# Performance work log

Hardware: AMD Instinct MI355X
Metric: run time of the kernel (lower is better)

The kernel has to match this reference:

```python
import jax, jax.numpy as jnp
import numpy as np

B, S, D, H = 4, 1024, 1024, 16
HD = D // H  # per-head dim = 64
NEG = -10000000000.0


def setup_inputs() -> dict:
    key = jax.random.key(0)
    ks = jax.random.split(key, 12)
    q = jax.random.normal(ks[0], (B, S, D), jnp.float32)
    k = jax.random.normal(ks[1], (B, S, D), jnp.float32)
    v = jax.random.normal(ks[2], (B, S, D), jnp.float32)
    mask = jax.random.randint(ks[3], (B, S, S), 0, 2).astype(jnp.int32)
    sc = 1.0 / np.sqrt(D)
    Wq = jax.random.normal(ks[4], (H, D, HD), jnp.float32) * sc
    bq = jnp.zeros((H, HD), jnp.float32)
    Wk = jax.random.normal(ks[5], (H, D, HD), jnp.float32) * sc
    bk = jnp.zeros((H, HD), jnp.float32)
    Wv = jax.random.normal(ks[6], (H, D, HD), jnp.float32) * sc
    bv = jnp.zeros((H, HD), jnp.float32)
    Wo = jax.random.normal(ks[7], (D, D), jnp.float32) * sc
    bo = jnp.zeros((D,), jnp.float32)
    return {"query": q, "key": k, "value": v, "attention_mask": mask,
            "Wq": Wq, "bq": bq, "Wk": Wk, "bk": bk, "Wv": Wv, "bv": bv,
            "Wo": Wo, "bo": bo}


def reference(query, key, value, attention_mask, Wq, bq, Wk, bk, Wv, bv, Wo, bo):
    # batched per-head projections: [B,S,D] x [H,D,E] -> [B,H,S,E]
    q = jnp.einsum('bsd,hde->bhse', query, Wq) + bq[None, :, None, :]
    k = jnp.einsum('bsd,hde->bhse', key, Wk) + bk[None, :, None, :]
    v = jnp.einsum('bsd,hde->bhse', value, Wv) + bv[None, :, None, :]
    # NOTE: scale uses key_dim (model_size = full D), faithful to source
    score = jnp.einsum('bhse,bhte->bhst', q, k) / jnp.sqrt(jnp.float32(D))
    m = attention_mask.astype(jnp.float32)[:, None, :, :]  # [B,1,S,S]
    score = score + (1.0 - m) * NEG
    attn = jax.nn.softmax(score, axis=-1) * m  # double masking
    heads = jnp.einsum('bhst,bhte->bhse', attn, v)  # [B,H,S,E]
    # concat heads along feature dim (head order preserved)
    heads = heads.transpose(0, 2, 1, 3).reshape(B, S, D)
    return heads @ Wo + bo
```

## Files before the change

### kernel.cpp

```cpp
#include <hip/hip_runtime.h>

#define B_ 4
#define S_ 1024
#define D_ 1024
#define H_ 16
#define E_ 64
#define BS_ (B_*S_)
#define BHSE_ (B_*H_*S_*E_)

typedef __attribute__((ext_vector_type(8))) short bf16x8;
typedef __attribute__((ext_vector_type(4))) float f32x4;
typedef __attribute__((ext_vector_type(4))) unsigned int u32x4;

__device__ __forceinline__ unsigned short f2bf(float f) {
    unsigned int x = __float_as_uint(f);
    x = (x + 0x7FFFu + ((x >> 16) & 1u)) >> 16;
    return (unsigned short)x;
}
__device__ __forceinline__ float bf2f(unsigned short u) {
    return __uint_as_float(((unsigned int)u) << 16);
}
__device__ __forceinline__ float ldin(const void* p, size_t i, int isb) {
    return isb ? bf2f(((const unsigned short*)p)[i]) : ((const float*)p)[i];
}

__device__ __forceinline__ unsigned int cvtpk(float lo, float hi) {
    unsigned int r;
    asm("v_cvt_pk_bf16_f32 %0, %1, %2" : "=v"(r) : "v"(lo), "v"(hi));
    return r;
}
__device__ __forceinline__ unsigned int bperm(int srclane4, unsigned int v) {
    return (unsigned int)__builtin_amdgcn_ds_bpermute(srclane4, (int)v);
}
__device__ __forceinline__ bf16x8 u4bf(u32x4 w) {
    union { u32x4 u; bf16x8 h; } c; c.u = w; return c.h;
}

#if __has_builtin(__builtin_amdgcn_exp2f)
#define EXP2(x) __builtin_amdgcn_exp2f(x)
#else
#define EXP2(x) __expf((x) * 0.6931471805599453f)
#endif

__device__ __forceinline__ void gl2lds16(const void* g, void* l) {
    __builtin_amdgcn_global_load_lds(
        (const __attribute__((address_space(1))) void*)g,
        (__attribute__((address_space(3))) void*)l, 16, 0, 0);
}

__device__ __forceinline__ int detect_isb(const unsigned int* q) {
    unsigned int wv = q[threadIdx.x & 63];
    unsigned int lo = wv & 0xFFFFu;
    unsigned int e = (lo >> 7) & 0xFFu;
    int ok = (lo == 0u) || (e >= 100u && e <= 145u);
    return __popcll(__ballot(ok)) >= 48;
}

__global__ __launch_bounds__(256) void preproc(
        const void* q_, const void* k_, const void* v_, const int* mask,
        const void* Wq, const void* Wk, const void* Wv, const void* Wo,
        const void* bq_, const void* bk_, const void* bv_, const void* bo_,
        unsigned short* WT, float* biases, unsigned long long* packT,
        unsigned short* Aconv) {
    __shared__ unsigned short Tt[64][72];
    const int isb = detect_isb((const unsigned int*)q_);
    const int blk = blockIdx.x, t = threadIdx.x;

    if (blk < 1024) {
        const int c0 = blk & 15, r0 = ((blk >> 4) & 15) * 64, z = blk >> 8;
        const void* src = (z == 0) ? Wq : (z == 1) ? Wk : (z == 2) ? Wv : Wo;
        {
            int dl = t >> 2, qc = t & 3;
            size_t base;
            if (z < 3) base = (size_t)c0 * 65536 + (size_t)(r0 + dl) * 64 + qc * 16;
            else       base = (size_t)(r0 + dl) * 1024 + (size_t)c0 * 64 + qc * 16;
            if (isb) {
                const unsigned short* s = (const unsigned short*)src + base;
                bf16x8 a0 = *(const bf16x8*)s, a1 = *(const bf16x8*)(s + 8);
#pragma unroll
                for (int j = 0; j < 8; j++) {
                    Tt[qc * 16 + j][dl] = (unsigned short)a0[j];
                    Tt[qc * 16 + 8 + j][dl] = (unsigned short)a1[j];
                }
            } else {
                const float* s = (const float*)src + base;
#pragma unroll
                for (int j = 0; j < 16; j++) Tt[qc * 16 + j][dl] = f2bf(s[j]);
            }
        }
        __syncthreads();
        {
            int el = t >> 2, qc = t & 3;
            size_t dst = (size_t)z * D_ * D_ + (size_t)(c0 * 64 + el) * D_ + r0 + qc * 16;
            *(bf16x8*)&WT[dst]     = *(const bf16x8*)&Tt[el][qc * 16];
            *(bf16x8*)&WT[dst + 8] = *(const bf16x8*)&Tt[el][qc * 16 + 8];
        }
        if (z == 3 && ((blk >> 4) & 15) == 0 && c0 < 4) {
            const void* bs = (c0 == 0) ? bq_ : (c0 == 1) ? bk_
                           : (c0 == 2) ? bv_ : bo_;
#pragma unroll
            for (int j = 0; j < 4; j++) {
                int i = t * 4 + j;
                biases[c0 * 1024 + i] = ldin(bs, i, isb);
            }
        }
    } else if (blk < 5120) {
        int unit = (blk - 1024) * 4 + (t >> 6);
        int lane = t & 63;
        int b = unit >> 12, rem = unit & 4095, s0 = (rem >> 4) * 4, kt = rem & 15;
        const int* mb = mask + ((size_t)b * 1024 + s0) * 1024 + kt * 64 + lane;
        unsigned long long bits[4];
#pragma unroll
        for (int j = 0; j < 4; j++) bits[j] = __ballot(mb[j * 1024] != 0);
        if (lane < 4) {
            unsigned long long bb = (lane == 0) ? bits[0] : (lane == 1) ? bits[1]
                                  : (lane == 2) ? bits[2] : bits[3];
            packT[((size_t)b * 16 + kt) * 1024 + s0 + lane] = bb;
        }
    } else {
        if (isb) return;
        int blk2 = blk - 5120;
        const int z = blk2 >> 11;
        const float* s = (z == 0) ? (const float*)q_ : (z == 1) ? (const float*)k_
                                                                : (const float*)v_;
        const size_t i = ((size_t)(blk2 & 2047) * 256 + t) * 8;
        f32x4 a0 = *(const f32x4*)(s + i);
        f32x4 a1 = *(const f32x4*)(s + i + 4);
        bf16x8 o;
#pragma unroll
        for (int j = 0; j < 4; j++) {
            o[j]     = (short)f2bf(a0[j]);
            o[4 + j] = (short)f2bf(a1[j]);
        }
        *(bf16x8*)&Aconv[(size_t)z * ((size_t)BS_ * D_) + i] = o;
    }
}

template<int BM, int BN, int MODE, int MINW>
__global__ __launch_bounds__(256, MINW) void gemm_k(
        const void* A0, const void* A1, const void* A2, const unsigned short* Aconv,
        const unsigned short* BtB, const float* biasB, void* dstB,
        const unsigned int* qdet) {
    constexpr int TOT16 = (BM + BN) * 32;
    constexpr int CALLS = TOT16 / 512;
    constexpr int CPW = CALLS / 4;
    constexpr int MT = BM / 32;
    constexpr int NT = BN / 32;
    __shared__ unsigned short buf[3][TOT16];

    const int fl = detect_isb(qdet);
    const int t = threadIdx.x, lane = t & 63, w = t >> 6;
    const int lm = lane & 15, q4 = lane >> 4;
    const int wm = w >> 1, wn = w & 1;
    const int lr = lane >> 2;
    const int ls = lane & 3;
    const int lg = ls ^ ((lr >> 1) & 3);

    const unsigned short* Abf;
    const unsigned short* Bt;
    const float* bias;
    int z = 0, m0, n0, phase;
    if (MODE == 0) {
        int bid = blockIdx.x + gridDim.x * (blockIdx.y + gridDim.y * blockIdx.z);
        int xcd = bid & 7, idx = bid >> 3;
        z = idx >> 5;
        int r = idx & 31;
        int mt = (xcd << 2) + (r & 3);
        int nt = r >> 2;
        m0 = mt * BM; n0 = nt * BN;
        phase = (nt * 13 + z * 5) & 31;
        const void* Ain = (z == 0) ? A0 : (z == 1 ? A1 : A2);
        Abf = fl ? (const unsigned short*)Ain
                 : Aconv + (size_t)z * ((size_t)BS_ * D_);
        Bt = BtB + (size_t)z * D_ * D_;
        bias = biasB + z * 1024;
    } else {
        Abf = (const unsigned short*)A0;
        Bt = BtB; bias = biasB;
        int bid = blockIdx.x + (blockIdx.y << 5);
        int xcd = bid & 7, idx = bid >> 3;
        m0 = ((xcd << 2) + (idx & 3)) * BM;
        n0 = (idx >> 2) * BN;
        phase = ((idx >> 2) * 13) & 31;
    }

    auto stage = [&](int kk, int bi) {
#pragma unroll
        for (int i = 0; i < CPW; ++i) {
            int c = w * CPW + i;
            int row = c * 16 + lr;
            const unsigned short* g;
            if (row < BM)
                g = Abf + (size_t)(m0 + row) * D_ + kk + lg * 8;
            else
                g = Bt + (size_t)(n0 + row - BM) * D_ + kk + lg * 8;
            gl2lds16(g, &buf[bi][c * 512]);
        }
    };

    f32x4 acc[MT][NT];
#pragma unroll
    for (int i = 0; i < MT; i++)
#pragma unroll
        for (int j = 0; j < NT; j++) acc[i][j] = (f32x4){0.f, 0.f, 0.f, 0.f};

    stage((phase & 31) * 32, 0);
    stage(((1 + phase) & 31) * 32, 1);
    for (int it = 0; it < D_ / 32; ++it) {
        const int bi = it % 3;
        if (it < D_ / 32 - 1) {
            asm volatile("s_waitcnt vmcnt(%0)" :: "n"(CPW) : "memory");
        } else {
            asm volatile("s_waitcnt vmcnt(0)" ::: "memory");
        }
        __builtin_amdgcn_s_barrier();
        __builtin_amdgcn_sched_barrier(0);
        if (it < D_ / 32 - 2) stage(((it + 2 + phase) & 31) * 32, (it + 2) % 3);

        const unsigned short* As = buf[bi];
        const unsigned short* Bs = buf[bi] + BM * 32;
        bf16x8 af[MT], bv[NT];
#pragma unroll
        for (int mt = 0; mt < MT; mt++) {
            int row = wm * (BM / 2) + mt * 16 + lm;
            af[mt] = *(const bf16x8*)&As[row * 32 + (q4 ^ ((row >> 1) & 3)) * 8];
        }
#pragma unroll
        for (int nt = 0; nt < NT; nt++) {
            int row = wn * (BN / 2) + nt * 16 + lm;
            bv[nt] = *(const bf16x8*)&Bs[row * 32 + (q4 ^ ((row >> 1) & 3)) * 8];
        }
#pragma unroll
        for (int mt = 0; mt < MT; mt++)
#pragma unroll
            for (int nt = 0; nt < NT; nt++)
                acc[mt][nt] = __builtin_amdgcn_mfma_f32_16x16x32_bf16(
                    af[mt], bv[nt], acc[mt][nt], 0, 0, 0);
    }

#pragma unroll
    for (int mt = 0; mt < MT; mt++)
#pragma unroll
        for (int nt = 0; nt < NT; nt++) {
            int N = n0 + wn * (BN / 2) + nt * 16 + lm;
            int Mb = m0 + wm * (BM / 2) + mt * 16 + q4 * 4;
            if (MODE == 0 && z == 2) {
                int bb = Mb >> 10, sb = Mb & 1023, hh = N >> 6, e = N & 63;
                unsigned long long hv = 0;
#pragma unroll
                for (int r = 0; r < 4; r++)
                    hv |= (unsigned long long)f2bf(acc[mt][nt][r] + bias[N]) << (16 * r);
                unsigned short* d16 = (unsigned short*)dstB + (size_t)2 * BHSE_;
                *(unsigned long long*)&d16[(((size_t)(bb * H_ + hh) * E_ + e) << 10) + sb] = hv;
            } else {
#pragma unroll
                for (int r = 0; r < 4; r++) {
                    int M = Mb + r;
                    float v = acc[mt][nt][r] + bias[N];
                    if (MODE == 0) {
                        int bb = M >> 10, s = M & 1023, hh = N >> 6, e = N & 63;
                        unsigned short* d16 = (unsigned short*)dstB + (size_t)z * BHSE_;
                        d16[((size_t)(bb * H_ + hh) * S_ + s) * E_ + e] = f2bf(v);
                    } else {
                        size_t idx = (size_t)M * D_ + N;
                        if (fl) ((unsigned short*)dstB)[idx] = f2bf(v);
                        else    ((float*)dstB)[idx] = v;
                    }
                }
            }
        }
}

__global__ __launch_bounds__(1024, 4) void attn64(
        const unsigned short* Qp, const unsigned short* Kp, const unsigned short* VpT,
        const unsigned long long* packT, unsigned short* heads) {
    __shared__ unsigned short KT[2][16384];
    __shared__ unsigned short VT[2][16384];

    const int bid = blockIdx.x + (blockIdx.y << 2) + (blockIdx.z << 6);
    const int xcd = bid & 7, idx = bid >> 3;
    const int qt = idx >> 3;
    const int hb = xcd * 8 + (idx & 7);
    const int h = hb & 15, b = hb >> 4;

    const int t = threadIdx.x, w = t >> 6, lane = t & 63, lm = lane & 15, q4 = lane >> 4;
    const size_t bh = ((size_t)b * H_ + h) * S_ * E_;
    const unsigned short* Qb = Qp + bh;
    const unsigned short* Kb = Kp + bh;
    const unsigned short* Vb = VpT + bh;
    const int q0 = qt * 256 + w * 16;

    const int l3 = lane >> 3, l7 = lane & 7;
    const int kLaneOff = l3 * 64 + (l7 ^ l3) * 8;
    const int vLaneOff = l3 * 1024 + (l7 ^ l3) * 8;

    const int sw = lm & 7;
    const int c0 = (q4 ^ sw) * 8, c1 = ((q4 ^ 4) ^ sw) * 8;

    const int srcA4 = ((lane & 15) | ((lane & 16) << 1)) << 2;
    const int srcB4 = srcA4 + 64;
    const bool selHi = (lane & 32) != 0;

    bf16x8 bq0 = *(const bf16x8*)&Qb[(size_t)(q0 + lm) * E_ + q4 * 8];
    bf16x8 bq1 = *(const bf16x8*)&Qb[(size_t)(q0 + lm) * E_ + 32 + q4 * 8];

    bf16x8 ones;
#pragma unroll
    for (int j = 0; j < 8; j++) ones[j] = (short)0x3F80;

    f32x4 oacc[4];
#pragma unroll
    for (int i = 0; i < 4; i++) oacc[i] = (f32x4){0.f, 0.f, 0.f, 0.f};
    f32x4 accL = (f32x4){0.f, 0.f, 0.f, 0.f};
    float mrun = -3.0e38f;
    const float scale2 = 0.03125f * 1.4426950408889634f;

#define STAGE(tile, bufi)                                                     \
    {                                                                         \
        int k0s = (tile) * 256;                                               \
        _Pragma("unroll")                                                     \
        for (int i_ = 0; i_ < 4; ++i_) {                                      \
            int c_ = w * 4 + i_;                                              \
            if (c_ < 32) {                                                    \
                gl2lds16(Kb + (size_t)k0s * 64 + c_ * 512 + kLaneOff,         \
                         &KT[bufi][c_ * 512]);                                \
            } else {                                                          \
                int cc_ = c_ - 32, sub_ = cc_ >> 3, ec_ = cc_ & 7;            \
                gl2lds16(Vb + (size_t)ec_ * 8192 + k0s + sub_ * 64 + vLaneOff,\
                         &VT[bufi][sub_ * 4096 + ec_ * 512]);                 \
            }                                                                 \
        }                                                                     \
    }

    STAGE(0, 0)
    unsigned long long mk[4], mkn[4];
#pragma unroll
    for (int j = 0; j < 4; j++)
        mk[j] = packT[((size_t)b * 16 + j) * 1024 + q0 + lm];

    for (int T = 0; T < S_ / 256; ++T) {
        const int bufi = T & 1;
        __syncthreads();
        if (T < 3) {
            STAGE(T + 1, bufi ^ 1)
#pragma unroll
            for (int j = 0; j < 4; j++)
                mkn[j] = packT[((size_t)b * 16 + 4 * T + 4 + j) * 1024 + q0 + lm];
        }

#pragma unroll
        for (int half = 0; half < 2; ++half) {
            f32x4 st[2][4];
            __builtin_amdgcn_s_setprio(1);
#pragma unroll
            for (int sub = 0; sub < 2; ++sub)
#pragma unroll
                for (int jt = 0; jt < 4; ++jt) {
                    const unsigned short* kr =
                        &KT[bufi][(half * 128 + sub * 64 + jt * 16 + lm) * 64];
                    bf16x8 ka0 = *(const bf16x8*)&kr[c0];
                    bf16x8 ka1 = *(const bf16x8*)&kr[c1];
                    f32x4 zz = (f32x4){0.f, 0.f, 0.f, 0.f};
                    zz = __builtin_amdgcn_mfma_f32_16x16x32_bf16(ka0, bq0, zz, 0, 0, 0);
                    zz = __builtin_amdgcn_mfma_f32_16x16x32_bf16(ka1, bq1, zz, 0, 0, 0);
                    st[sub][jt] = zz;
                }
            __builtin_amdgcn_s_setprio(0);

            float tmx = -3.0e38f;
#pragma unroll
            for (int sub = 0; sub < 2; ++sub)
#pragma unroll
                for (int jt = 0; jt < 4; ++jt) {
                    float a = fmaxf(st[sub][jt][0], st[sub][jt][1]);
                    float c = fmaxf(st[sub][jt][2], st[sub][jt][3]);
                    tmx = fmaxf(tmx, fmaxf(a, c));
                }
            float pmax = tmx * scale2;

            if (!__all(pmax - mrun <= 8.f)) {
                float rmx = pmax;
                rmx = fmaxf(rmx, __shfl_xor(rmx, 16, 64));
                rmx = fmaxf(rmx, __shfl_xor(rmx, 32, 64));
                float mnew = fmaxf(mrun, rmx);
                float alpha = EXP2(mrun - mnew);
                accL = accL * alpha;
#pragma unroll
                for (int nt = 0; nt < 4; nt++) oacc[nt] = oacc[nt] * alpha;
                mrun = mnew;
            }
            const float mneg = -mrun;

            unsigned int cl[2][8];
#pragma unroll
            for (int sub = 0; sub < 2; ++sub) {
                unsigned long long mkv = mk[half * 2 + sub];
                unsigned int mn = (unsigned int)(mkv >> (q4 * 4));
                unsigned int mh = (unsigned int)(mkv >> (q4 * 4 + 32));
#pragma unroll
                for (int jt = 0; jt < 4; ++jt) {
                    unsigned int mm = (jt & 2) ? mh : mn;
                    const int sh = (jt & 1) * 16;
                    float p0 = EXP2(fmaf(st[sub][jt][0], scale2, mneg));
                    float p1 = EXP2(fmaf(st[sub][jt][1], scale2, mneg));
                    float p2 = EXP2(fmaf(st[sub][jt][2], scale2, mneg));
                    float p3 = EXP2(fmaf(st[sub][jt][3], scale2, mneg));
                    p0 = (mm & (1u << (sh + 0))) ? p0 : 0.f;
                    p1 = (mm & (1u << (sh + 1))) ? p1 : 0.f;
                    p2 = (mm & (1u << (sh + 2))) ? p2 : 0.f;
                    p3 = (mm & (1u << (sh + 3))) ? p3 : 0.f;
                    cl[sub][jt * 2]     = cvtpk(p0, p1);
                    cl[sub][jt * 2 + 1] = cvtpk(p2, p3);
                }
            }

#pragma unroll
            for (int sub = 0; sub < 2; ++sub) {
                unsigned int* c = cl[sub];
                u32x4 w0, w1;
                {
                    unsigned int aA0 = bperm(srcA4, c[0]), aA2 = bperm(srcA4, c[2]);
                    unsigned int aA1 = bperm(srcA4, c[1]), aA3 = bperm(srcA4, c[3]);
                    unsigned int aB0 = bperm(srcB4, c[0]), aB2 = bperm(srcB4, c[2]);
                    unsigned int aB1 = bperm(srcB4, c[1]), aB3 = bperm(srcB4, c[3]);
                    w0 = (u32x4){selHi ? aA2 : aA0, selHi ? aA3 : aA1,
                                 selHi ? aB2 : aB0, selHi ? aB3 : aB1};
                    unsigned int bA0 = bperm(srcA4, c[4]), bA2 = bperm(srcA4, c[6]);
                    unsigned int bA1 = bperm(srcA4, c[5]), bA3 = bperm(srcA4, c[7]);
                    unsigned int bB0 = bperm(srcB4, c[4]), bB2 = bperm(srcB4, c[6]);
                    unsigned int bB1 = bperm(srcB4, c[5]), bB3 = bperm(srcB4, c[7]);
                    w1 = (u32x4){selHi ? bA2 : bA0, selHi ? bA3 : bA1,
                                 selHi ? bB2 : bB0, selHi ? bB3 : bB1};
                }
                bf16x8 bp0 = u4bf(w0);
                bf16x8 bp1 = u4bf(w1);

                __builtin_amdgcn_s_setprio(1);
                accL = __builtin_amdgcn_mfma_f32_16x16x32_bf16(ones, bp0, accL, 0, 0, 0);
                accL = __builtin_amdgcn_mfma_f32_16x16x32_bf16(ones, bp1, accL, 0, 0, 0);

                const unsigned short* vbase = &VT[bufi][(half * 2 + sub) * 4096];
#pragma unroll
                for (int nt = 0; nt < 4; nt++) {
                    const unsigned short* vr = &vbase[(nt * 16 + lm) * 64];
                    bf16x8 va0 = *(const bf16x8*)&vr[c0];
                    bf16x8 va1 = *(const bf16x8*)&vr[c1];
                    oacc[nt] = __builtin_amdgcn_mfma_f32_16x16x32_bf16(va0, bp0, oacc[nt], 0, 0, 0);
                    oacc[nt] = __builtin_amdgcn_mfma_f32_16x16x32_bf16(va1, bp1, oacc[nt], 0, 0, 0);
                }
                __builtin_amdgcn_s_setprio(0);
            }
        }

#pragma unroll
        for (int j = 0; j < 4; j++) mk[j] = mkn[j];
    }

    float inv = 1.0f / accL[0];
#pragma unroll
    for (int nt = 0; nt < 4; nt++) {
        unsigned int lo = cvtpk(oacc[nt][0] * inv, oacc[nt][1] * inv);
        unsigned int hi = cvtpk(oacc[nt][2] * inv, oacc[nt][3] * inv);
        unsigned long long hv = (unsigned long long)lo | ((unsigned long long)hi << 32);
        *(unsigned long long*)&heads[(size_t)(b * S_ + q0 + lm) * D_ + h * E_ + nt * 16 + q4 * 4] = hv;
    }
}

extern "C" void kernel_launch(void* const* d_in, const int* in_sizes, int n_in,
                              void* d_out, int out_size, void* d_ws, size_t ws_size,
                              hipStream_t stream) {
    char* ws = (char*)d_ws;
    unsigned short* WT = (unsigned short*)(ws + 256);
    unsigned short* WqT = WT;
    unsigned short* WoT = WT + (size_t)3 * D_ * D_;
    float* biases = (float*)(WT + (size_t)4 * D_ * D_);
    float* bq = biases;
    float* bo = biases + 3 * 1024;
    unsigned short* Qp = (unsigned short*)(biases + 4 * 1024);
    unsigned short* Kp = Qp + (size_t)BHSE_;
    unsigned short* Vp = Kp + (size_t)BHSE_;
    unsigned short* heads = Vp + (size_t)BHSE_;
    unsigned long long* packT = (unsigned long long*)(heads + (size_t)BHSE_);
    unsigned short* Aconv = (unsigned short*)(packT + (size_t)B_ * 16 * S_);

    preproc<<<11264, 256, 0, stream>>>(
        d_in[0], d_in[1], d_in[2], (const int*)d_in[3],
        d_in[4], d_in[6], d_in[8], d_in[10],
        d_in[5], d_in[7], d_in[9], d_in[11],
        WT, biases, packT, Aconv);
    gemm_k<128, 128, 0, 3><<<dim3(32, 8, 3), 256, 0, stream>>>(
        d_in[0], d_in[1], d_in[2], Aconv, WqT, bq, Qp,
        (const unsigned int*)d_in[0]);
    attn64<<<dim3(4, 16, 4), 1024, 0, stream>>>(Qp, Kp, Vp, packT, heads);
    gemm_k<128, 64, 1, 4><<<dim3(32, 16, 1), 256, 0, stream>>>(
        heads, nullptr, nullptr, nullptr, WoT, bo, d_out,
        (const unsigned int*)d_in[0]);
}
```

Baseline: 219.9 us.

## Replace QKV projection GEMM with 256x256-tile 8-wave pipelined kernel

Adds a dedicated QKV projection kernel that uses 256x256 output tiles and 512 threads (8 waves, 128x64 each). It double-buffers the K dimension in 32-wide halves with interleaved global-to-LDS staging, explicit vmcnt waits, sched barriers and setprio around the MFMA bursts. Each block's K loop starts at a rotated offset. The goal is more data reuse per LDS load and better overlap of memory with MFMA work. The trade-off is a 192-block grid that is close to one wave on the CU count, and high register pressure from the 32 accumulators per wave.

```diff
diff --git a/kernel.cpp b/kernel.cpp
--- a/kernel.cpp
+++ b/kernel.cpp
@@ -136,10 +136,138 @@
     }
 }
 
-template<int BM, int BN, int MODE, int MINW>
-__global__ __launch_bounds__(256, MINW) void gemm_k(
+__global__ __launch_bounds__(512, 2) void proj8(
         const void* A0, const void* A1, const void* A2, const unsigned short* Aconv,
         const unsigned short* BtB, const float* biasB, void* dstB,
+        const unsigned int* qdet) {
+    __shared__ unsigned short lds[2][2][2][16][512];
+
+    const int fl = detect_isb(qdet);
+    const int t = threadIdx.x, lane = t & 63, w = t >> 6;
+    const int lm = lane & 15, q4 = lane >> 4;
+    const int wm = w >> 2, wn = w & 3;
+    const int lr = lane >> 2;
+    const int ls = lane & 3;
+    const int lg = ls ^ ((lr >> 1) & 3);
+
+    const int bid = blockIdx.x;
+    const int xcd = bid & 7, idx = bid >> 3;
+    const int z = idx >> 3;
+    const int r = idx & 7;
+    const int m0 = (xcd * 2 + (r & 1)) * 256;
+    const int n0 = (r >> 1) * 256;
+    const int rot = ((r >> 1) * 5 + z * 3) & 15;
+
+    const void* Ain = (z == 0) ? A0 : (z == 1 ? A1 : A2);
+    const unsigned short* Abf = fl ? (const unsigned short*)Ain
+                                   : Aconv + (size_t)z * ((size_t)BS_ * D_);
+    const unsigned short* Bt = BtB + (size_t)z * D_ * D_;
+    const float* bias = biasB + z * 1024;
+
+    auto stageHalf = [&](int T, int kh, int ab) {
+        int kbase = ((T + rot) & 15) * 64 + kh * 32;
+        unsigned short* dst = &lds[T & 1][kh][ab][0][0];
+#pragma unroll
+        for (int i2 = 0; i2 < 2; ++i2) {
+            int c = w * 2 + i2;
+            const unsigned short* g = (ab == 0)
+                ? Abf + (size_t)(m0 + c * 16 + lr) * D_ + kbase + lg * 8
+                : Bt + (size_t)(n0 + c * 16 + lr) * D_ + kbase + lg * 8;
+            gl2lds16(g, dst + c * 512);
+        }
+    };
+    auto ldA = [&](int buf, int kh, int mh, bf16x8* af) {
+        const unsigned short* As = &lds[buf][kh][0][0][0];
+#pragma unroll
+        for (int f = 0; f < 4; f++) {
+            int row = wm * 128 + mh * 64 + f * 16 + lm;
+            af[f] = *(const bf16x8*)&As[row * 32 + (q4 ^ ((row >> 1) & 3)) * 8];
+        }
+    };
+    auto ldB = [&](int buf, int kh, bf16x8* bv) {
+        const unsigned short* Bs = &lds[buf][kh][1][0][0];
+#pragma unroll
+        for (int n = 0; n < 4; n++) {
+            int row = wn * 64 + n * 16 + lm;
+            bv[n] = *(const bf16x8*)&Bs[row * 32 + (q4 ^ ((row >> 1) & 3)) * 8];
+        }
+    };
+
+    f32x4 acc[8][4];
+#pragma unroll
+    for (int i = 0; i < 8; i++)
+#pragma unroll
+        for (int j = 0; j < 4; j++) acc[i][j] = (f32x4){0.f, 0.f, 0.f, 0.f};
+
+    stageHalf(0, 0, 0); stageHalf(0, 0, 1);
+    stageHalf(0, 1, 0); stageHalf(0, 1, 1);
+    stageHalf(1, 0, 0); stageHalf(1, 0, 1);
+
+    bf16x8 af[4], bv[4];
+
+#define PHASE(BUF, KH, MH, NEWK, ST, SKH, SAB, VM)                            \
+    {                                                                         \
+        if (VM) asm volatile("s_waitcnt vmcnt(8)" ::: "memory");              \
+        asm volatile("s_barrier" ::: "memory");                               \
+        __builtin_amdgcn_sched_barrier(0);                                    \
+        if (NEWK) ldB(BUF, KH, bv);                                           \
+        ldA(BUF, KH, MH, af);                                                 \
+        stageHalf(ST, SKH, SAB);                                              \
+        __builtin_amdgcn_s_setprio(1);                                        \
+        _Pragma("unroll")                                                     \
+        for (int f = 0; f < 4; f++)                                           \
+            _Pragma("unroll")                                                 \
+            for (int n = 0; n < 4; n++)                                       \
+                acc[MH * 4 + f][n] = __builtin_amdgcn_mfma_f32_16x16x32_bf16( \
+                    af[f], bv[n], acc[MH * 4 + f][n], 0, 0, 0);               \
+        __builtin_amdgcn_s_setprio(0);                                        \
+        __builtin_amdgcn_sched_barrier(0);                                    \
+    }
+
+    for (int i = 0; i < 8; ++i) {
+        const int a = 2 * i, b = 2 * i + 1;
+        PHASE(0, 0, 0, 1, b,     1, 0, 1)
+        PHASE(0, 0, 1, 0, b,     1, 1, 0)
+        PHASE(0, 1, 0, 1, a + 2, 0, 0, 1)
+        PHASE(0, 1, 1, 0, a + 2, 0, 1, 0)
+        PHASE(1, 0, 0, 1, a + 2, 1, 0, 1)
+        PHASE(1, 0, 1, 0, a + 2, 1, 1, 0)
+        PHASE(1, 1, 0, 1, b + 2, 0, 0, 1)
+        PHASE(1, 1, 1, 0, b + 2, 0, 1, 0)
+    }
+#undef PHASE
+    asm volatile("s_waitcnt vmcnt(0)" ::: "memory");
+
+#pragma unroll
+    for (int mf = 0; mf < 8; mf++)
+#pragma unroll
+        for (int nf = 0; nf < 4; nf++) {
+            int N = n0 + wn * 64 + nf * 16 + lm;
+            int Mb = m0 + wm * 128 + mf * 16 + q4 * 4;
+            if (z == 2) {
+                int bb = Mb >> 10, sb = Mb & 1023, hh = N >> 6, e = N & 63;
+                unsigned long long hv = 0;
+#pragma unroll
+                for (int rr = 0; rr < 4; rr++)
+                    hv |= (unsigned long long)f2bf(acc[mf][nf][rr] + bias[N]) << (16 * rr);
+                unsigned short* d16 = (unsigned short*)dstB + (size_t)2 * BHSE_;
+                *(unsigned long long*)&d16[(((size_t)(bb * H_ + hh) * E_ + e) << 10) + sb] = hv;
+            } else {
+#pragma unroll
+                for (int rr = 0; rr < 4; rr++) {
+                    int M = Mb + rr;
+                    float v = acc[mf][nf][rr] + bias[N];
+                    int bb = M >> 10, s = M & 1023, hh = N >> 6, e = N & 63;
+                    unsigned short* d16 = (unsigned short*)dstB + (size_t)z * BHSE_;
+                    d16[((size_t)(bb * H_ + hh) * S_ + s) * E_ + e] = f2bf(v);
+                }
+            }
+        }
+}
+
+template<int BM, int BN, int MINW>
+__global__ __launch_bounds__(256, MINW) void gemm_k(
+        const void* A0, const unsigned short* BtB, const float* biasB, void* dstB,
         const unsigned int* qdet) {
     constexpr int TOT16 = (BM + BN) * 32;
     constexpr int CALLS = TOT16 / 512;
@@ -156,33 +284,14 @@
     const int ls = lane & 3;
     const int lg = ls ^ ((lr >> 1) & 3);
 
-    const unsigned short* Abf;
-    const unsigned short* Bt;
-    const float* bias;
-    int z = 0, m0, n0, phase;
-    if (MODE == 0) {
-        int bid = blockIdx.x + gridDim.x * (blockIdx.y + gridDim.y * blockIdx.z);
-        int xcd = bid & 7, idx = bid >> 3;
-        z = idx >> 5;
-        int r = idx & 31;
-        int mt = (xcd << 2) + (r & 3);
-        int nt = r >> 2;
-        m0 = mt * BM; n0 = nt * BN;
-        phase = (nt * 13 + z * 5) & 31;
-        const void* Ain = (z == 0) ? A0 : (z == 1 ? A1 : A2);
-        Abf = fl ? (const unsigned short*)Ain
-                 : Aconv + (size_t)z * ((size_t)BS_ * D_);
-        Bt = BtB + (size_t)z * D_ * D_;
-        bias = biasB + z * 1024;
-    } else {
-        Abf = (const unsigned short*)A0;
-        Bt = BtB; bias = biasB;
-        int bid = blockIdx.x + (blockIdx.y << 5);
-        int xcd = bid & 7, idx = bid >> 3;
-        m0 = ((xcd << 2) + (idx & 3)) * BM;
-        n0 = (idx >> 2) * BN;
-        phase = ((idx >> 2) * 13) & 31;
-    }
+    const unsigned short* Abf = (const unsigned short*)A0;
+    const unsigned short* Bt = BtB;
+    const float* bias = biasB;
+    int bid = blockIdx.x + (blockIdx.y << 5);
+    int xcd = bid & 7, idx = bid >> 3;
+    int m0 = ((xcd << 2) + (idx & 3)) * BM;
+    int n0 = (idx >> 2) * BN;
+    int phase = ((idx >> 2) * 13) & 31;
 
     auto stage = [&](int kk, int bi) {
 #pragma unroll
@@ -244,29 +353,13 @@
         for (int nt = 0; nt < NT; nt++) {
             int N = n0 + wn * (BN / 2) + nt * 16 + lm;
             int Mb = m0 + wm * (BM / 2) + mt * 16 + q4 * 4;
-            if (MODE == 0 && z == 2) {
-                int bb = Mb >> 10, sb = Mb & 1023, hh = N >> 6, e = N & 63;
-                unsigned long long hv = 0;
-#pragma unroll
-                for (int r = 0; r < 4; r++)
-                    hv |= (unsigned long long)f2bf(acc[mt][nt][r] + bias[N]) << (16 * r);
-                unsigned short* d16 = (unsigned short*)dstB + (size_t)2 * BHSE_;
-                *(unsigned long long*)&d16[(((size_t)(bb * H_ + hh) * E_ + e) << 10) + sb] = hv;
-            } else {
-#pragma unroll
-                for (int r = 0; r < 4; r++) {
-                    int M = Mb + r;
-                    float v = acc[mt][nt][r] + bias[N];
-                    if (MODE == 0) {
-                        int bb = M >> 10, s = M & 1023, hh = N >> 6, e = N & 63;
-                        unsigned short* d16 = (unsigned short*)dstB + (size_t)z * BHSE_;
-                        d16[((size_t)(bb * H_ + hh) * S_ + s) * E_ + e] = f2bf(v);
-                    } else {
-                        size_t idx = (size_t)M * D_ + N;
-                        if (fl) ((unsigned short*)dstB)[idx] = f2bf(v);
-                        else    ((float*)dstB)[idx] = v;
-                    }
-                }
+#pragma unroll
+            for (int rr = 0; rr < 4; rr++) {
+                int M = Mb + rr;
+                float v = acc[mt][nt][rr] + bias[N];
+                size_t oidx = (size_t)M * D_ + N;
+                if (fl) ((unsigned short*)dstB)[oidx] = f2bf(v);
+                else    ((float*)dstB)[oidx] = v;
             }
         }
 }
@@ -488,11 +581,10 @@
         d_in[4], d_in[6], d_in[8], d_in[10],
         d_in[5], d_in[7], d_in[9], d_in[11],
         WT, biases, packT, Aconv);
-    gemm_k<128, 128, 0, 3><<<dim3(32, 8, 3), 256, 0, stream>>>(
+    proj8<<<192, 512, 0, stream>>>(
         d_in[0], d_in[1], d_in[2], Aconv, WqT, bq, Qp,
         (const unsigned int*)d_in[0]);
     attn64<<<dim3(4, 16, 4), 1024, 0, stream>>>(Qp, Kp, Vp, packT, heads);
-    gemm_k<128, 64, 1, 4><<<dim3(32, 16, 1), 256, 0, stream>>>(
-        heads, nullptr, nullptr, nullptr, WoT, bo, d_out,
-        (const unsigned int*)d_in[0]);
-}
+    gemm_k<128, 64, 4><<<dim3(32, 16, 1), 256, 0, stream>>>(
+        heads, WoT, bo, d_out, (const unsigned int*)d_in[0]);
+}
```

Result: no change. 220.2 us (+0.1%).
